# Optimization experiments

Measured on AMD Instinct MI355X. Metric: run time of the kernel, lower is better.

The kernel has to match this reference:

```python
import jax, jax.numpy as jnp
import numpy as np

B, C, U, V, H, W = 4, 64, 5, 5, 64, 64
MID = 64  # mid_dim defaults to dim


def setup_inputs() -> dict:
    key = jax.random.key(0)
    ks = jax.random.split(key, 13)
    s = 0.05
    inp = {"x": jax.random.normal(ks[0], (B, C, U, V, H, W), dtype=jnp.float32)}
    # body: Conv2d(dim->mid,1x1), SiLU, Conv2d(mid->dim,1x1)
    inp["w1"] = jax.random.normal(ks[1], (MID, C), dtype=jnp.float32) * s
    inp["b1"] = jax.random.normal(ks[2], (MID,), dtype=jnp.float32) * s
    inp["w2"] = jax.random.normal(ks[3], (C, MID), dtype=jnp.float32) * s
    inp["b2"] = jax.random.normal(ks[4], (C,), dtype=jnp.float32) * s
    # four fuse 1x1 convs (dim->dim)
    for i in range(4):
        inp[f"fw{i}"] = jax.random.normal(ks[5 + 2 * i], (C, C), dtype=jnp.float32) * s
        inp[f"fb{i}"] = jax.random.normal(ks[6 + 2 * i], (C,), dtype=jnp.float32) * s
    return inp


def _conv1x1(w, b, x):
    # x: (B,C,h,w); w: (O,C); 1x1 conv == channel matmul
    return jnp.einsum('oc,bchw->bohw', w, x) + b[None, :, None, None]


def reference(x, w1, b1, w2, b2, fw0, fb0, fw1, fb1, fw2, fb2, fw3, fb3):
    # Four 2-axis mean pools over the 6D tensor
    hw_m = x.mean(axis=(2, 3))   # (B,C,H,W)
    uv_m = x.mean(axis=(4, 5))   # (B,C,U,V)
    uh_m = x.mean(axis=(3, 5))   # (B,C,U,H)
    vw_m = x.mean(axis=(2, 4))   # (B,C,V,W)
    # Assemble padded buffer uvhw of shape (B,C,H+V,W+U)
    top = jnp.concatenate([hw_m, jnp.swapaxes(uh_m, -1, -2)], axis=-1)  # (B,C,H,W+U)
    bot = jnp.concatenate([vw_m, jnp.swapaxes(uv_m, -1, -2)], axis=-1)  # (B,C,V,W+U)
    uvhw = jnpp_concat = jnp.concatenate([top, bot], axis=-2)           # (B,C,H+V,W+U)
    # body: conv1x1 -> SiLU -> conv1x1
    uvhw = _conv1x1(w2, b2, jax.nn.silu(_conv1x1(w1, b1, uvhw)))
    # Split back into the four pooled maps
    hw = uvhw[..., :H, :W]
    vw = uvhw[..., H:, :W]
    uh = jnp.swapaxes(uvhw[..., :H, W:], -1, -2)  # (B,C,U,H)
    uv = jnp.swapaxes(uvhw[..., H:, W:], -1, -2)  # (B,C,U,V)
    # Per-branch fuse convs, then broadcast-gate x and sum
    hw = _conv1x1(fw0, fb0, hw).reshape(B, C, 1, 1, H, W)
    uv = _conv1x1(fw1, fb1, uv).reshape(B, C, U, V, 1, 1)
    uh = _conv1x1(fw2, fb2, uh).reshape(B, C, U, 1, H, 1)
    vw = _conv1x1(fw3, fb3, vw).reshape(B, C, 1, V, 1, W)
    return x * hw + x * uv + x * uh + x * vw
```

## Files before the change

### kernel.cpp

```cpp
#include <hip/hip_runtime.h>
#include <hip/hip_bf16.h>
#include <cstddef>

#define BB 4
#define CC 64
#define UU 5
#define VV 5
#define HH 64
#define WW 64

typedef float f4v __attribute__((ext_vector_type(4)));

__device__ __forceinline__ float rdlane(float v, int l) {
    return __uint_as_float((unsigned)__builtin_amdgcn_readlane((int)__float_as_uint(v), l));
}
__device__ __forceinline__ float rfl(float v) {
    return __uint_as_float((unsigned)__builtin_amdgcn_readfirstlane((int)__float_as_uint(v)));
}
__device__ __forceinline__ float sum4(float4 a) { return (a.x+a.y)+(a.z+a.w); }
__device__ __forceinline__ void nt_store4(float4 r, float4* p) {
    union { float4 s; f4v v; } u; u.s = r;
    __builtin_nontemporal_store(u.v, (f4v*)p);
}

__global__ __launch_bounds__(256) void k1_means(const float* __restrict__ x,
        float* __restrict__ m_hw, float* __restrict__ R,
        float* __restrict__ vw_part) {
    const int bid  = blockIdx.x;
    const int bc   = bid >> 1;
    const int half = bid & 1;
    const int t    = threadIdx.x;
    const int wave = t >> 6;
    const int lane = t & 63;

    const float4* xs = (const float4*)x + (size_t)bc * 25600
                     + (size_t)half * 512;

    __shared__ float smem[25*512];

    float4 hwacc[2];
    hwacc[0] = make_float4(0.f,0.f,0.f,0.f);
    hwacc[1] = make_float4(0.f,0.f,0.f,0.f);
    float4 vwacc[5];
    #pragma unroll
    for (int v = 0; v < 5; ++v) vwacc[v] = make_float4(0.f,0.f,0.f,0.f);

    #pragma unroll
    for (int u = 0; u < 5; ++u) {
        #pragma unroll
        for (int v = 0; v < 5; ++v) {
            const int k = u*5 + v;
            #pragma unroll
            for (int r = 0; r < 2; ++r) {
                float4 q = xs[(size_t)k*1024 + r*256 + t];
                hwacc[r].x += q.x; hwacc[r].y += q.y;
                hwacc[r].z += q.z; hwacc[r].w += q.w;
                vwacc[v].x += q.x; vwacc[v].y += q.y;
                vwacc[v].z += q.z; vwacc[v].w += q.w;
                smem[k*512 + r*256 + t] = sum4(q);
            }
        }
    }

    #pragma unroll
    for (int r = 0; r < 2; ++r) {
        float4 o;
        o.x = hwacc[r].x*(1.f/25.f); o.y = hwacc[r].y*(1.f/25.f);
        o.z = hwacc[r].z*(1.f/25.f); o.w = hwacc[r].w*(1.f/25.f);
        ((float4*)m_hw)[(size_t)bc*1024 + half*512 + r*256 + t] = o;
    }

    __syncthreads();

    for (int task = t; task < 800; task += 256) {
        const int k    = task >> 5;
        const int hloc = task & 31;
        const float* row = &smem[k*512 + hloc*16];
        float s = 0.f;
        #pragma unroll
        for (int j = 0; j < 16; ++j) s += row[j];
        R[((size_t)bc*25 + k)*64 + half*32 + hloc] = s;
    }
    __syncthreads();

    float4* vwbuf = (float4*)smem;
    #pragma unroll
    for (int v = 0; v < 5; ++v) {
        float4 s = vwacc[v];
        s.x += __shfl_xor(s.x, 16); s.y += __shfl_xor(s.y, 16);
        s.z += __shfl_xor(s.z, 16); s.w += __shfl_xor(s.w, 16);
        s.x += __shfl_xor(s.x, 32); s.y += __shfl_xor(s.y, 32);
        s.z += __shfl_xor(s.z, 32); s.w += __shfl_xor(s.w, 32);
        if (lane < 16) vwbuf[(wave*5 + v)*16 + lane] = s;
    }
    __syncthreads();

    if (t < 80) {
        const int v = t >> 4;
        float4 s = vwbuf[(0*5 + v)*16 + (t & 15)];
        #pragma unroll
        for (int w4 = 1; w4 < 4; ++w4) {
            float4 pp = vwbuf[(w4*5 + v)*16 + (t & 15)];
            s.x += pp.x; s.y += pp.y; s.z += pp.z; s.w += pp.w;
        }
        ((float4*)vw_part)[(size_t)bid*80 + t] = s;
    }
}

#define LOADROW(dst, src)                                              \
    { _Pragma("unroll")                                                \
      for (int q = 0; q < 16; ++q) {                                   \
          float4 t4 = ((const float4*)(src))[lane*16 + q];             \
          dst[4*q+0] = t4.x; dst[4*q+1] = t4.y;                        \
          dst[4*q+2] = t4.z; dst[4*q+3] = t4.w;                        \
      } }

#define DOT64(res, wr, src)                                            \
    float res;                                                         \
    { float _a0=0.f,_a1=0.f,_a2=0.f,_a3=0.f;                           \
      _Pragma("unroll")                                                \
      for (int cc2 = 0; cc2 < 64; cc2 += 4) {                          \
          _a0 = fmaf(wr[cc2+0], rdlane(src, cc2+0), _a0);              \
          _a1 = fmaf(wr[cc2+1], rdlane(src, cc2+1), _a1);              \
          _a2 = fmaf(wr[cc2+2], rdlane(src, cc2+2), _a2);              \
          _a3 = fmaf(wr[cc2+3], rdlane(src, cc2+3), _a3);              \
      }                                                                \
      res = (_a0 + _a1) + (_a2 + _a3); }

#define MLP_CORE(VIN, OUTEXPR)                                         \
    {                                                                  \
        float v = (VIN);                                               \
        DOT64(d1, w1r, v);                                             \
        float acc1 = d1 + b1v;                                         \
        float ya = acc1 / (1.f + __expf(-acc1));                       \
        DOT64(d2, w2r, ya);                                            \
        float acc2 = d2 + b2v;                                         \
        DOT64(d3, fr, acc2);                                           \
        OUTEXPR = d3 + fbv;                                            \
    }

__global__ __launch_bounds__(64, 1) void k2_mlp(
        const float* __restrict__ m_hw, const float* __restrict__ R,
        const float* __restrict__ vw_part,
        const float* __restrict__ w1, const float* __restrict__ b1,
        const float* __restrict__ w2, const float* __restrict__ b2,
        const float* __restrict__ fw0, const float* __restrict__ fb0,
        const float* __restrict__ fw1, const float* __restrict__ fb1,
        const float* __restrict__ fw2, const float* __restrict__ fb2,
        const float* __restrict__ fw3, const float* __restrict__ fb3,
        float* __restrict__ mod_hw, float* __restrict__ mod_uh,
        float* __restrict__ mod_vw, float* __restrict__ mod_uv) {
    const int blk  = blockIdx.x;
    const int row  = blk >> 2;
    const int chnk = blk & 3;
    const int b    = row / 69;
    const int i    = row % 69;
    const int lane = threadIdx.x & 63;

    const int j0 = chnk * 18;
    const int j1 = min(69, j0 + 18);
    const bool top = (i < 64);

    const float* fwA = top ? fw0 : fw3;
    const float* fbA = top ? fb0 : fb3;
    const float* fwB = top ? fw2 : fw1;
    const float* fbB = top ? fb2 : fb1;

    float w1r[64], w2r[64], fr[64];
    LOADROW(w1r, w1);
    LOADROW(w2r, w2);
    const float b1v = b1[lane];
    const float b2v = b2[lane];

    const int b64c = b * CC + lane;
    const int cbl  = b64c;

    const int jm = min(j1, 64);
    if (j0 < jm) {
        LOADROW(fr, fwA);
        const float fbv = fbA[lane];
        if (top) {
            const float* src = m_hw + (size_t)b64c*4096 + i*64;
            float* sp = mod_hw + ((size_t)cbl*64 + i)*64;
            for (int j = j0; j < jm; ++j)
                MLP_CORE(src[j], sp[j])
        } else {
            const float* q0 = vw_part + ((size_t)b64c*2 + 0)*320 + (i-64)*64;
            const float* q1 = vw_part + ((size_t)b64c*2 + 1)*320 + (i-64)*64;
            float* sp = mod_vw + (size_t)cbl*320 + (i-64)*64;
            for (int j = j0; j < jm; ++j)
                MLP_CORE((q0[j] + q1[j]) * (1.f/320.f), sp[j])
        }
    }
    if (j1 > 64) {
        LOADROW(fr, fwB);
        const float fbv = fbB[lane];
        const int jb = max(j0, 64);
        if (top) {
            float* sp = mod_uh + (size_t)cbl*320 + i;
            for (int j = jb; j < j1; ++j) {
                const int u = j - 64;
                const float* Rp = R + ((size_t)b64c*25 + u*5)*64 + i;
                float vin = (Rp[0] + Rp[64] + Rp[128] + Rp[192] + Rp[256])
                            * (1.f/320.f);
                MLP_CORE(vin, sp[(size_t)u*64])
            }
        } else {
            float* sp = mod_uv + (size_t)cbl*25 + (i-64);
            for (int j = jb; j < j1; ++j) {
                const int u = j - 64;
                const float4* Rp4 = (const float4*)(R
                    + ((size_t)b64c*25 + u*5 + (i-64))*64);
                float4 a = make_float4(0.f,0.f,0.f,0.f);
                #pragma unroll
                for (int k = 0; k < 16; ++k) {
                    float4 pp = Rp4[k];
                    a.x += pp.x; a.y += pp.y; a.z += pp.z; a.w += pp.w;
                }
                MLP_CORE(sum4(a) * (1.f/4096.f), sp[(size_t)u*5])
            }
        }
    }
}

__global__ __launch_bounds__(256, 4) void k3_apply(
        const float* __restrict__ x,
        const float* __restrict__ mod_hw, const float* __restrict__ mod_uh,
        const float* __restrict__ mod_vw, const float* __restrict__ mod_uv,
        float* __restrict__ out) {
    const int blk  = blockIdx.x;
    const int bc   = blk >> 2;
    const int qt   = blk & 3;
    const int t    = threadIdx.x;
    const int base = qt*256 + t;
    const int h    = base >> 4;

    float4 mh = ((const float4*)(mod_hw + (size_t)bc * 4096))[base];
    float uh[5];
    #pragma unroll
    for (int u = 0; u < 5; ++u) uh[u] = mod_uh[(size_t)bc*320 + u*64 + h];
    float4 vw[5];
    #pragma unroll
    for (int v = 0; v < 5; ++v)
        vw[v] = ((const float4*)(mod_vw + (size_t)bc*320 + v*64))[t & 15];
    float uv[25];
    #pragma unroll
    for (int k = 0; k < 25; ++k)
        uv[k] = rfl(mod_uv[(size_t)bc*25 + k]);

    const float4* x4 = (const float4*)(x + (size_t)bc * (UU*VV*HH*WW));
    float4* o4 = (float4*)(out + (size_t)bc * (UU*VV*HH*WW));

    #pragma unroll
    for (int u = 0; u < 5; ++u) {
        #pragma unroll
        for (int v = 0; v < 5; ++v) {
            const int idx = (u*5 + v)*1024 + base;
            float4 xv = x4[idx];
            const float s = uh[u] + uv[u*5 + v];
            float4 r;
            r.x = xv.x * (mh.x + vw[v].x + s);
            r.y = xv.y * (mh.y + vw[v].y + s);
            r.z = xv.z * (mh.z + vw[v].z + s);
            r.w = xv.w * (mh.w + vw[v].w + s);
            nt_store4(r, &o4[idx]);
        }
    }
}

extern "C" void kernel_launch(void* const* d_in, const int* in_sizes, int n_in,
                              void* d_out, int out_size, void* d_ws, size_t ws_size,
                              hipStream_t stream) {
    const float* x   = (const float*)d_in[0];
    const float* w1  = (const float*)d_in[1];
    const float* b1  = (const float*)d_in[2];
    const float* w2  = (const float*)d_in[3];
    const float* b2  = (const float*)d_in[4];
    const float* fw0 = (const float*)d_in[5];
    const float* fb0 = (const float*)d_in[6];
    const float* fw1 = (const float*)d_in[7];
    const float* fb1 = (const float*)d_in[8];
    const float* fw2 = (const float*)d_in[9];
    const float* fb2 = (const float*)d_in[10];
    const float* fw3 = (const float*)d_in[11];
    const float* fb3 = (const float*)d_in[12];

    float* ws = (float*)d_ws;
    float* mod_hw = ws;
    float* mod_uh = mod_hw + 1048576;
    float* mod_vw = mod_uh + 81920;
    float* mod_uv = mod_vw + 81920;

    float* m_hw    = (float*)d_out;
    float* Rbuf    = m_hw + 1048576;
    float* vw_part = Rbuf + 409600;

    k1_means<<<BB*CC*2, 256, 0, stream>>>(x, m_hw, Rbuf, vw_part);
    k2_mlp<<<BB*69*4, 64, 0, stream>>>(m_hw, Rbuf, vw_part, w1, b1, w2, b2,
                                       fw0, fb0, fw1, fb1, fw2, fb2, fw3, fb3,
                                       mod_hw, mod_uh, mod_vw, mod_uv);
    k3_apply<<<BB*CC*4, 256, 0, stream>>>(x, mod_hw, mod_uh, mod_vw, mod_uv,
                                          (float*)d_out);
}
```

Before: 99.76 us.

## Fuse means, MLP and apply kernels into one cooperative kernel with grid syncs

Replaces the three-kernel pipeline (means, per-row MLP, apply) with a single cooperative kernel of 256 blocks × 512 threads, separated by two grid.sync barriers. Each block handles one (b,c) slice for the reduction and apply phases. Each wave takes one MLP task, indexed by wave*256+block. The aim is to remove two kernel launch boundaries and their tail and drain gaps. The cost is lower occupancy in the bandwidth-bound phases, possible register spills in the MLP phase under the 512-thread launch bound, and extra host-side attribute and occupancy queries on every call. The original three launches remain as a fallback if the cooperative launch fails.

New measurement: 100.4 us. About the same (+0.7%).

```diff
diff --git a/kernel.cpp b/kernel.cpp
--- a/kernel.cpp
+++ b/kernel.cpp
@@ -1,6 +1,9 @@
 #include <hip/hip_runtime.h>
+#include <hip/hip_cooperative_groups.h>
 #include <hip/hip_bf16.h>
 #include <cstddef>
+
+namespace cg = cooperative_groups;
 
 #define BB 4
 #define CC 64
@@ -21,6 +24,254 @@
 __device__ __forceinline__ void nt_store4(float4 r, float4* p) {
     union { float4 s; f4v v; } u; u.s = r;
     __builtin_nontemporal_store(u.v, (f4v*)p);
+}
+
+#define LOADROW(dst, src)                                              \
+    { _Pragma("unroll")                                                \
+      for (int q = 0; q < 16; ++q) {                                   \
+          float4 t4 = ((const float4*)(src))[lane*16 + q];             \
+          dst[4*q+0] = t4.x; dst[4*q+1] = t4.y;                        \
+          dst[4*q+2] = t4.z; dst[4*q+3] = t4.w;                        \
+      } }
+
+#define DOT64(res, wr, src)                                            \
+    float res;                                                         \
+    { float _a0=0.f,_a1=0.f,_a2=0.f,_a3=0.f;                           \
+      _Pragma("unroll")                                                \
+      for (int cc2 = 0; cc2 < 64; cc2 += 4) {                          \
+          _a0 = fmaf(wr[cc2+0], rdlane(src, cc2+0), _a0);              \
+          _a1 = fmaf(wr[cc2+1], rdlane(src, cc2+1), _a1);              \
+          _a2 = fmaf(wr[cc2+2], rdlane(src, cc2+2), _a2);              \
+          _a3 = fmaf(wr[cc2+3], rdlane(src, cc2+3), _a3);              \
+      }                                                                \
+      res = (_a0 + _a1) + (_a2 + _a3); }
+
+#define MLP_CORE(VIN, OUTEXPR)                                         \
+    {                                                                  \
+        float v = (VIN);                                               \
+        DOT64(d1, w1r, v);                                             \
+        float acc1 = d1 + b1v;                                         \
+        float ya = acc1 / (1.f + __expf(-acc1));                       \
+        DOT64(d2, w2r, ya);                                            \
+        float acc2 = d2 + b2v;                                         \
+        DOT64(d3, fr, acc2);                                           \
+        OUTEXPR = d3 + fbv;                                            \
+    }
+
+#define K2_BODY(WTASK)                                                 \
+    {                                                                  \
+        const int row  = (WTASK) >> 2;                                 \
+        const int chnk = (WTASK) & 3;                                  \
+        const int b    = row / 69;                                     \
+        const int i    = row % 69;                                     \
+        const int j0 = chnk * 18;                                      \
+        const int j1 = min(69, j0 + 18);                               \
+        const bool top = (i < 64);                                     \
+        const float* fwA = top ? fw0 : fw3;                            \
+        const float* fbA = top ? fb0 : fb3;                            \
+        const float* fwB = top ? fw2 : fw1;                            \
+        const float* fbB = top ? fb2 : fb1;                            \
+        float w1r[64], w2r[64], fr[64];                                \
+        LOADROW(w1r, w1);                                              \
+        LOADROW(w2r, w2);                                              \
+        const float b1v = b1[lane];                                    \
+        const float b2v = b2[lane];                                    \
+        const int b64c = b * CC + lane;                                \
+        const int cbl  = b64c;                                         \
+        const int jm = min(j1, 64);                                    \
+        if (j0 < jm) {                                                 \
+            LOADROW(fr, fwA);                                          \
+            const float fbv = fbA[lane];                               \
+            if (top) {                                                 \
+                const float* src = m_hw + (size_t)b64c*4096 + i*64;    \
+                float* sp = mod_hw + ((size_t)cbl*64 + i)*64;          \
+                for (int j = j0; j < jm; ++j)                          \
+                    MLP_CORE(src[j], sp[j])                            \
+            } else {                                                   \
+                const float* q0 = vw_part + ((size_t)b64c*2 + 0)*320 + (i-64)*64; \
+                const float* q1 = vw_part + ((size_t)b64c*2 + 1)*320 + (i-64)*64; \
+                float* sp = mod_vw + (size_t)cbl*320 + (i-64)*64;      \
+                for (int j = j0; j < jm; ++j)                          \
+                    MLP_CORE((q0[j] + q1[j]) * (1.f/320.f), sp[j])     \
+            }                                                          \
+        }                                                              \
+        if (j1 > 64) {                                                 \
+            LOADROW(fr, fwB);                                          \
+            const float fbv = fbB[lane];                               \
+            const int jb = max(j0, 64);                                \
+            if (top) {                                                 \
+                float* sp = mod_uh + (size_t)cbl*320 + i;              \
+                for (int j = jb; j < j1; ++j) {                        \
+                    const int u = j - 64;                              \
+                    const float* Rp = R + ((size_t)b64c*25 + u*5)*64 + i; \
+                    float vin = (Rp[0] + Rp[64] + Rp[128] + Rp[192] + Rp[256]) \
+                                * (1.f/320.f);                         \
+                    MLP_CORE(vin, sp[(size_t)u*64])                    \
+                }                                                      \
+            } else {                                                   \
+                float* sp = mod_uv + (size_t)cbl*25 + (i-64);          \
+                for (int j = jb; j < j1; ++j) {                        \
+                    const int u = j - 64;                              \
+                    const float4* Rp4 = (const float4*)(R              \
+                        + ((size_t)b64c*25 + u*5 + (i-64))*64);        \
+                    float4 a = make_float4(0.f,0.f,0.f,0.f);           \
+                    _Pragma("unroll")                                  \
+                    for (int k = 0; k < 16; ++k) {                     \
+                        float4 pp = Rp4[k];                            \
+                        a.x += pp.x; a.y += pp.y; a.z += pp.z; a.w += pp.w; \
+                    }                                                  \
+                    MLP_CORE(sum4(a) * (1.f/4096.f), sp[(size_t)u*5])  \
+                }                                                      \
+            }                                                          \
+        }                                                              \
+    }
+
+__global__ __launch_bounds__(512, 2) void fused_all(
+        const float* __restrict__ x,
+        float* __restrict__ m_hw, float* __restrict__ R,
+        float* __restrict__ vw_part,
+        const float* __restrict__ w1, const float* __restrict__ b1,
+        const float* __restrict__ w2, const float* __restrict__ b2,
+        const float* __restrict__ fw0, const float* __restrict__ fb0,
+        const float* __restrict__ fw1, const float* __restrict__ fb1,
+        const float* __restrict__ fw2, const float* __restrict__ fb2,
+        const float* __restrict__ fw3, const float* __restrict__ fb3,
+        float* __restrict__ mod_hw, float* __restrict__ mod_uh,
+        float* __restrict__ mod_vw, float* __restrict__ mod_uv,
+        float* __restrict__ out) {
+    cg::grid_group grid = cg::this_grid();
+    const int blk  = blockIdx.x;
+    const int t    = threadIdx.x;
+    const int wave = t >> 6;
+    const int lane = t & 63;
+
+    __shared__ float smem[25*512];
+
+    const int bc = blk;
+    #pragma unroll 1
+    for (int hi = 0; hi < 2; ++hi) {
+        if (hi) __syncthreads();
+        const int bid = bc*2 + hi;
+        const float4* xs = (const float4*)x + (size_t)bc * 25600
+                         + (size_t)hi * 512;
+
+        float4 hw = make_float4(0.f,0.f,0.f,0.f);
+        float4 vwacc[5];
+        #pragma unroll
+        for (int v = 0; v < 5; ++v) vwacc[v] = make_float4(0.f,0.f,0.f,0.f);
+
+        #pragma unroll
+        for (int u = 0; u < 5; ++u) {
+            #pragma unroll
+            for (int v = 0; v < 5; ++v) {
+                const int k = u*5 + v;
+                float4 q = xs[(size_t)k*1024 + t];
+                hw.x += q.x; hw.y += q.y; hw.z += q.z; hw.w += q.w;
+                vwacc[v].x += q.x; vwacc[v].y += q.y;
+                vwacc[v].z += q.z; vwacc[v].w += q.w;
+                smem[k*512 + t] = sum4(q);
+            }
+        }
+
+        float4 o;
+        o.x = hw.x*(1.f/25.f); o.y = hw.y*(1.f/25.f);
+        o.z = hw.z*(1.f/25.f); o.w = hw.w*(1.f/25.f);
+        ((float4*)m_hw)[(size_t)bc*1024 + hi*512 + t] = o;
+
+        __syncthreads();
+
+        for (int task = t; task < 800; task += 512) {
+            const int k    = task >> 5;
+            const int hloc = task & 31;
+            const float* row = &smem[k*512 + hloc*16];
+            float s = 0.f;
+            #pragma unroll
+            for (int j = 0; j < 16; ++j) s += row[j];
+            R[((size_t)bc*25 + k)*64 + hi*32 + hloc] = s;
+        }
+        __syncthreads();
+
+        float4* vwbuf = (float4*)smem;
+        #pragma unroll
+        for (int v = 0; v < 5; ++v) {
+            float4 s = vwacc[v];
+            s.x += __shfl_xor(s.x, 16); s.y += __shfl_xor(s.y, 16);
+            s.z += __shfl_xor(s.z, 16); s.w += __shfl_xor(s.w, 16);
+            s.x += __shfl_xor(s.x, 32); s.y += __shfl_xor(s.y, 32);
+            s.z += __shfl_xor(s.z, 32); s.w += __shfl_xor(s.w, 32);
+            if (lane < 16) vwbuf[(wave*5 + v)*16 + lane] = s;
+        }
+        __syncthreads();
+
+        if (t < 80) {
+            const int v = t >> 4;
+            float4 s = vwbuf[(0*5 + v)*16 + (t & 15)];
+            #pragma unroll
+            for (int w8 = 1; w8 < 8; ++w8) {
+                float4 pp = vwbuf[(w8*5 + v)*16 + (t & 15)];
+                s.x += pp.x; s.y += pp.y; s.z += pp.z; s.w += pp.w;
+            }
+            ((float4*)vw_part)[(size_t)bid*80 + t] = s;
+        }
+    }
+
+    grid.sync();
+
+    {
+        const int wt = wave*256 + blk;
+        if (wt < 1104) K2_BODY(wt)
+    }
+
+    grid.sync();
+
+    {
+        float4 mh0 = ((const float4*)(mod_hw + (size_t)bc * 4096))[t];
+        float4 mh1 = ((const float4*)(mod_hw + (size_t)bc * 4096))[512 + t];
+        const int h0 = t >> 4;
+        const int h1 = 32 + h0;
+        float uh0[5], uh1[5];
+        #pragma unroll
+        for (int u = 0; u < 5; ++u) {
+            uh0[u] = mod_uh[(size_t)bc*320 + u*64 + h0];
+            uh1[u] = mod_uh[(size_t)bc*320 + u*64 + h1];
+        }
+        float4 vw[5];
+        #pragma unroll
+        for (int v = 0; v < 5; ++v)
+            vw[v] = ((const float4*)(mod_vw + (size_t)bc*320 + v*64))[t & 15];
+        float uv[25];
+        #pragma unroll
+        for (int k = 0; k < 25; ++k)
+            uv[k] = rfl(mod_uv[(size_t)bc*25 + k]);
+
+        const float4* x4 = (const float4*)(x + (size_t)bc * (UU*VV*HH*WW));
+        float4* o4 = (float4*)(out + (size_t)bc * (UU*VV*HH*WW));
+
+        #pragma unroll
+        for (int u = 0; u < 5; ++u) {
+            #pragma unroll
+            for (int v = 0; v < 5; ++v) {
+                const int k = u*5 + v;
+                const int idx0 = k*1024 + t;
+                const int idx1 = idx0 + 512;
+                float4 xv0 = x4[idx0];
+                float4 xv1 = x4[idx1];
+                const float s0 = uh0[u] + uv[k];
+                const float s1 = uh1[u] + uv[k];
+                float4 r0, r1;
+                r0.x = xv0.x * (mh0.x + vw[v].x + s0);
+                r0.y = xv0.y * (mh0.y + vw[v].y + s0);
+                r0.z = xv0.z * (mh0.z + vw[v].z + s0);
+                r0.w = xv0.w * (mh0.w + vw[v].w + s0);
+                r1.x = xv1.x * (mh1.x + vw[v].x + s1);
+                r1.y = xv1.y * (mh1.y + vw[v].y + s1);
+                r1.z = xv1.z * (mh1.z + vw[v].z + s1);
+                r1.w = xv1.w * (mh1.w + vw[v].w + s1);
+                nt_store4(r0, &o4[idx0]);
+                nt_store4(r1, &o4[idx1]);
+            }
+        }
+    }
 }
 
 __global__ __launch_bounds__(256) void k1_means(const float* __restrict__ x,
@@ -106,38 +357,6 @@
         ((float4*)vw_part)[(size_t)bid*80 + t] = s;
     }
 }
-
-#define LOADROW(dst, src)                                              \
-    { _Pragma("unroll")                                                \
-      for (int q = 0; q < 16; ++q) {                                   \
-          float4 t4 = ((const float4*)(src))[lane*16 + q];             \
-          dst[4*q+0] = t4.x; dst[4*q+1] = t4.y;                        \
-          dst[4*q+2] = t4.z; dst[4*q+3] = t4.w;                        \
-      } }
-
-#define DOT64(res, wr, src)                                            \
-    float res;                                                         \
-    { float _a0=0.f,_a1=0.f,_a2=0.f,_a3=0.f;                           \
-      _Pragma("unroll")                                                \
-      for (int cc2 = 0; cc2 < 64; cc2 += 4) {                          \
-          _a0 = fmaf(wr[cc2+0], rdlane(src, cc2+0), _a0);              \
-          _a1 = fmaf(wr[cc2+1], rdlane(src, cc2+1), _a1);              \
-          _a2 = fmaf(wr[cc2+2], rdlane(src, cc2+2), _a2);              \
-          _a3 = fmaf(wr[cc2+3], rdlane(src, cc2+3), _a3);              \
-      }                                                                \
-      res = (_a0 + _a1) + (_a2 + _a3); }
-
-#define MLP_CORE(VIN, OUTEXPR)                                         \
-    {                                                                  \
-        float v = (VIN);                                               \
-        DOT64(d1, w1r, v);                                             \
-        float acc1 = d1 + b1v;                                         \
-        float ya = acc1 / (1.f + __expf(-acc1));                       \
-        DOT64(d2, w2r, ya);                                            \
-        float acc2 = d2 + b2v;                                         \
-        DOT64(d3, fr, acc2);                                           \
-        OUTEXPR = d3 + fbv;                                            \
-    }
 
 __global__ __launch_bounds__(64, 1) void k2_mlp(
         const float* __restrict__ m_hw, const float* __restrict__ R,
@@ -151,76 +370,8 @@
         float* __restrict__ mod_hw, float* __restrict__ mod_uh,
         float* __restrict__ mod_vw, float* __restrict__ mod_uv) {
     const int blk  = blockIdx.x;
-    const int row  = blk >> 2;
-    const int chnk = blk & 3;
-    const int b    = row / 69;
-    const int i    = row % 69;
     const int lane = threadIdx.x & 63;
-
-    const int j0 = chnk * 18;
-    const int j1 = min(69, j0 + 18);
-    const bool top = (i < 64);
-
-    const float* fwA = top ? fw0 : fw3;
-    const float* fbA = top ? fb0 : fb3;
-    const float* fwB = top ? fw2 : fw1;
-    const float* fbB = top ? fb2 : fb1;
-
-    float w1r[64], w2r[64], fr[64];
-    LOADROW(w1r, w1);
-    LOADROW(w2r, w2);
-    const float b1v = b1[lane];
-    const float b2v = b2[lane];
-
-    const int b64c = b * CC + lane;
-    const int cbl  = b64c;
-
-    const int jm = min(j1, 64);
-    if (j0 < jm) {
-        LOADROW(fr, fwA);
-        const float fbv = fbA[lane];
-        if (top) {
-            const float* src = m_hw + (size_t)b64c*4096 + i*64;
-            float* sp = mod_hw + ((size_t)cbl*64 + i)*64;
-            for (int j = j0; j < jm; ++j)
-                MLP_CORE(src[j], sp[j])
-        } else {
-            const float* q0 = vw_part + ((size_t)b64c*2 + 0)*320 + (i-64)*64;
-            const float* q1 = vw_part + ((size_t)b64c*2 + 1)*320 + (i-64)*64;
-            float* sp = mod_vw + (size_t)cbl*320 + (i-64)*64;
-            for (int j = j0; j < jm; ++j)
-                MLP_CORE((q0[j] + q1[j]) * (1.f/320.f), sp[j])
-        }
-    }
-    if (j1 > 64) {
-        LOADROW(fr, fwB);
-        const float fbv = fbB[lane];
-        const int jb = max(j0, 64);
-        if (top) {
-            float* sp = mod_uh + (size_t)cbl*320 + i;
-            for (int j = jb; j < j1; ++j) {
-                const int u = j - 64;
-                const float* Rp = R + ((size_t)b64c*25 + u*5)*64 + i;
-                float vin = (Rp[0] + Rp[64] + Rp[128] + Rp[192] + Rp[256])
-                            * (1.f/320.f);
-                MLP_CORE(vin, sp[(size_t)u*64])
-            }
-        } else {
-            float* sp = mod_uv + (size_t)cbl*25 + (i-64);
-            for (int j = jb; j < j1; ++j) {
-                const int u = j - 64;
-                const float4* Rp4 = (const float4*)(R
-                    + ((size_t)b64c*25 + u*5 + (i-64))*64);
-                float4 a = make_float4(0.f,0.f,0.f,0.f);
-                #pragma unroll
-                for (int k = 0; k < 16; ++k) {
-                    float4 pp = Rp4[k];
-                    a.x += pp.x; a.y += pp.y; a.z += pp.z; a.w += pp.w;
-                }
-                MLP_CORE(sum4(a) * (1.f/4096.f), sp[(size_t)u*5])
-            }
-        }
-    }
+    K2_BODY(blk)
 }
 
 __global__ __launch_bounds__(256, 4) void k3_apply(
@@ -294,6 +445,32 @@
     float* m_hw    = (float*)d_out;
     float* Rbuf    = m_hw + 1048576;
     float* vw_part = Rbuf + 409600;
+    float* outp    = (float*)d_out;
+
+    int dev = 0;
+    hipGetDevice(&dev);
+    int coop = 0;
+    hipDeviceGetAttribute(&coop, hipDeviceAttributeCooperativeLaunch, dev);
+    int maxb = 0;
+    hipError_t occ_err = hipOccupancyMaxActiveBlocksPerMultiprocessor(
+        &maxb, (const void*)fused_all, 512, 0);
+    bool use_coop = (coop != 0) && (occ_err == hipSuccess) && (maxb >= 1);
+
+    if (use_coop) {
+        void* args[] = {
+            (void*)&x, (void*)&m_hw, (void*)&Rbuf, (void*)&vw_part,
+            (void*)&w1, (void*)&b1, (void*)&w2, (void*)&b2,
+            (void*)&fw0, (void*)&fb0, (void*)&fw1, (void*)&fb1,
+            (void*)&fw2, (void*)&fb2, (void*)&fw3, (void*)&fb3,
+            (void*)&mod_hw, (void*)&mod_uh, (void*)&mod_vw, (void*)&mod_uv,
+            (void*)&outp
+        };
+        hipError_t err = hipLaunchCooperativeKernel((const void*)fused_all,
+                                                    dim3(256), dim3(512),
+                                                    args, 0, stream);
+        if (err == hipSuccess) return;
+        (void)hipGetLastError();
+    }
 
     k1_means<<<BB*CC*2, 256, 0, stream>>>(x, m_hw, Rbuf, vw_part);
     k2_mlp<<<BB*69*4, 64, 0, stream>>>(m_hw, Rbuf, vw_part, w1, b1, w2, b2,
```
